# Kernel optimization log

Measured on AMD Instinct MI355X. Metric: run time of the kernel, lower is better.

The kernel has to match this reference:

```python
import jax, jax.numpy as jnp
import numpy as np

B, N, CS, CV, K = 8, 2048, 256, 128, 3
EPS = 1e-6


def _eq_layernorm(s, v):
    # scalars: standard layernorm over channels; vectors: RMS of channel norms (equivariant)
    mu = s.mean(-1, keepdims=True)
    var = ((s - mu) ** 2).mean(-1, keepdims=True)
    s = (s - mu) * jax.lax.rsqrt(var + EPS)
    n2 = (v ** 2).sum(-1).mean(-1, keepdims=True)  # [b,n,1]
    v = v * jax.lax.rsqrt(n2 + EPS)[..., None]
    return s, v


def setup_inputs() -> dict:
    key = jax.random.key(0)
    ks = jax.random.split(key, 7)
    fan_s = K * (CS + CV)       # 1152
    fan_v = K * (CS + 2 * CV)   # 1536
    return {
        "x_s": jax.random.normal(ks[0], (B, N, CS), jnp.float32),
        "x_v": jax.random.normal(ks[1], (B, N, CV, 3), jnp.float32),
        "coords": jax.random.normal(ks[2], (B, N, 3), jnp.float32) * 10.0,
        "W_conv_s": jax.random.normal(ks[3], (fan_s, CS), jnp.float32),
        "W_conv_v": jax.random.normal(ks[4], (fan_v, CV), jnp.float32),
        "W_si_s": jax.random.normal(ks[5], (CS, CS), jnp.float32),
        "W_si_v": jax.random.normal(ks[6], (CV, CV), jnp.float32),
    }


def reference(x_s, x_v, coords, W_conv_s, W_conv_v, W_si_s, W_si_v):
    b, n, cs = x_s.shape
    cv = x_v.shape[2]
    pad = K // 2
    # 'same' padding: zeros for features, edge for coords (zero displacement at boundary)
    sp = jnp.pad(x_s, ((0, 0), (pad, pad), (0, 0)))
    vp = jnp.pad(x_v, ((0, 0), (pad, pad), (0, 0), (0, 0)))
    cp = jnp.pad(coords, ((0, 0), (pad, pad), (0, 0)), mode="edge")
    s_win = jnp.stack([sp[:, k:k + n] for k in range(K)], 2)   # [b,n,K,cs]
    v_win = jnp.stack([vp[:, k:k + n] for k in range(K)], 2)   # [b,n,K,cv,3]
    c_win = jnp.stack([cp[:, k:k + n] for k in range(K)], 2)   # [b,n,K,3]

    d = c_win - coords[:, :, None, :]
    dn = jnp.linalg.norm(d, axis=-1, keepdims=True)
    rhat = d * jnp.where(dn > 1e-6, 1.0 / jnp.maximum(dn, 1e-6), 0.0)

    # Clebsch-Gordan paths of (0e,1e) features with sh = (1, rhat)
    vdot = jnp.einsum("bnkcd,bnkd->bnkc", v_win, rhat)                    # 1x1 -> 0
    scal_in = jnp.concatenate([s_win, vdot], -1).reshape(b, n, -1)        # [b,n,K*(cs+cv)]
    s_rhat = s_win[..., None] * rhat[:, :, :, None, :]                    # 0x1 -> 1
    v_cross = jnp.cross(v_win, rhat[:, :, :, None, :])                    # 1x1 -> 1
    vec_in = jnp.concatenate([v_win, s_rhat, v_cross], 3).reshape(b, n, -1, 3)

    # SequenceConvolution linear mixing (fan-in normalized) + norm=True
    h_s = jnp.einsum("bnp,po->bno", scal_in, W_conv_s) / float(np.sqrt(scal_in.shape[-1]))
    h_v = jnp.einsum("bnpd,po->bnod", vec_in, W_conv_v) / float(np.sqrt(vec_in.shape[2]))
    h_s, h_v = _eq_layernorm(h_s, h_v)

    # SelfInteraction: per-degree channel mixing, residual=True, norm_last=True
    y_s = h_s + h_s @ W_si_s / float(np.sqrt(cs))
    y_v = h_v + jnp.einsum("bncd,co->bnod", h_v, W_si_v) / float(np.sqrt(cv))
    y_s, y_v = _eq_layernorm(y_s, y_v)

    # block Residual + final EquivariantLayerNorm
    z_s, z_v = _eq_layernorm(x_s + y_s, x_v + y_v)
    return z_s, z_v
```

## Files before the change

kernel.cpp:

```cpp
#include <hip/hip_runtime.h>
#include <hip/hip_bf16.h>


typedef __attribute__((ext_vector_type(8))) short short8;
typedef __attribute__((ext_vector_type(4))) float f32x4;
typedef unsigned short u16;

#define B_   8
#define N_   2048
#define EPS_ 1e-6f
#define TB   64

#define OFF_CS 0
#define OFF_V  294912
#define OFF_G  393216
#define OFF_SS 491520
#define OFF_SV 557056

#define MFMA(a,b,c) __builtin_amdgcn_mfma_f32_16x16x32_bf16((a),(b),(c),0,0,0)

__device__ __forceinline__ u16 f2b(float v){ __hip_bfloat16 h=__float2bfloat16(v); return *(u16*)&h; }

__global__ __launch_bounds__(256) void prep_weights(
    const float* __restrict__ Wcs, const float* __restrict__ Wcv,
    const float* __restrict__ Wss, const float* __restrict__ Wsv,
    u16* __restrict__ ws)
{
    const int bid = blockIdx.x;
    const float* src; int N, r0, ld, c0; u16* dst; int tile;
    if (bid < 288)      { src=Wcs; N=256; r0=0; dst=ws+OFF_CS; ld=1152; c0=0; tile=bid; }
    else if (bid < 336) { int k=(bid-288)/16; tile=(bid-288)%16;
                          src=Wcv; N=128; r0=k*512;     dst=ws+OFF_V; ld=768; c0=k*256; }
    else if (bid < 432) { int k=(bid-336)/32; tile=(bid-336)%32;
                          src=Wcv; N=128; r0=k*512+128; dst=ws+OFF_G; ld=768; c0=k*256; }
    else if (bid < 480) { int k=(bid-432)/16; tile=(bid-432)%16;
                          src=Wcv; N=128; r0=k*512+384; dst=ws+OFF_V; ld=768; c0=k*256+128; }
    else if (bid < 544) { tile=bid-480; src=Wss; N=256; r0=0; dst=ws+OFF_SS; ld=256; c0=0; }
    else                { tile=bid-544; src=Wsv; N=128; r0=0; dst=ws+OFF_SV; ld=128; c0=0; }
    const int ntN = N >> 5;
    const int kt = (tile/ntN)*32, nn = (tile%ntN)*32;
    __shared__ float t[32][33];
    const int r = threadIdx.x >> 5, c = threadIdx.x & 31;
#pragma unroll
    for (int i = 0; i < 4; ++i)
        t[r+8*i][c] = src[(size_t)(r0+kt+r+8*i)*N + nn+c];
    __syncthreads();
#pragma unroll
    for (int i = 0; i < 4; ++i)
        dst[(size_t)(nn+r+8*i)*ld + c0+kt+c] = f2b(t[c][r+8*i]);
}

__device__ __forceinline__ void ln_reduce(
    float p1[4][4], float p2[4][4], float pv[4][4], f32x4* red,
    int lm, int lq4, int w, float mu[4][4], float ss[4][4], float vs[4][4])
{
    __syncthreads();
#pragma unroll
    for (int m2 = 1; m2 < 16; m2 <<= 1)
#pragma unroll
        for (int m = 0; m < 4; ++m)
#pragma unroll
            for (int q = 0; q < 4; ++q) {
                p1[m][q] += __shfl_xor(p1[m][q], m2);
                p2[m][q] += __shfl_xor(p2[m][q], m2);
                pv[m][q] += __shfl_xor(pv[m][q], m2);
            }
    if (lm == 0)
#pragma unroll
        for (int m = 0; m < 4; ++m)
#pragma unroll
            for (int q = 0; q < 4; ++q) {
                f32x4 r = {p1[m][q], p2[m][q], pv[m][q], 0.f};
                red[(m*16+lq4+q)*8 + w] = r;
            }
    __syncthreads();
#pragma unroll
    for (int m = 0; m < 4; ++m)
#pragma unroll
        for (int q = 0; q < 4; ++q) {
            const int t = m*16 + lq4 + q;
            f32x4 rs = red[t*8+0];
#pragma unroll
            for (int i = 1; i < 8; ++i) rs += red[t*8+i];
            const float mm = rs.x * (1.f/256.f);
            mu[m][q] = mm;
            ss[m][q] = rsqrtf(rs.y*(1.f/256.f) - mm*mm + EPS_);
            vs[m][q] = rsqrtf(rs.z*(1.f/128.f) + EPS_);
        }
}

__global__ __launch_bounds__(512, 2) void mixing_main(
    const float* __restrict__ x_s, const float* __restrict__ x_v,
    const float* __restrict__ coords, const u16* __restrict__ wt,
    float* __restrict__ out)
{
    __shared__ __align__(16) char smem[162816];
    u16*   fs  = (u16*)smem;
    u16*   fv  = (u16*)(smem + 50176);
    u16*   hsb = (u16*)smem;
    u16*   hvb = (u16*)(smem + 50176);
    float* xvL = (float*)(smem + 50176);
    float* rhp = (float*)(smem + 151552);
    f32x4* red = (f32x4*)(smem + 154624);

    const int tid = threadIdx.x;
    const int w   = tid >> 6, l = tid & 63;
    const int lm  = l & 15, lk8 = (l >> 4) << 3, lq4 = (l >> 4) << 2;
    const int gt0 = blockIdx.x * TB;
    const int n0  = gt0 & (N_ - 1);
    const int seq0 = gt0 - n0;
    const size_t ZV0 = (size_t)B_ * N_ * 256;

    if (tid < 192) {
        const int t = tid / 3, k = tid - 3 * (tid / 3);
        const int jn = n0 + t + k - 1;
        const int jc = jn < 0 ? 0 : (jn > N_-1 ? N_-1 : jn);
        const float* cj = coords + (size_t)(seq0 + jc) * 3;
        const float* c0p = coords + (size_t)(gt0 + t) * 3;
        const float d0 = cj[0]-c0p[0], d1 = cj[1]-c0p[1], d2 = cj[2]-c0p[2];
        const float dn = sqrtf(d0*d0 + d1*d1 + d2*d2);
        const float inv = dn > 1e-6f ? 1.f/dn : 0.f;
        rhp[(t*3+k)*4+0] = d0*inv; rhp[(t*3+k)*4+1] = d1*inv; rhp[(t*3+k)*4+2] = d2*inv;
    }
    __syncthreads();

    const f32x4 fz = {0.f,0.f,0.f,0.f};
    f32x4 acc_s[4][2];
    f32x4 accv[12];
#pragma unroll
    for (int m = 0; m < 4; ++m) { acc_s[m][0] = fz; acc_s[m][1] = fz; }
#pragma unroll
    for (int mi = 0; mi < 12; ++mi) accv[mi] = fz;

    const int bt = tid >> 3;
    const int bx = tid & 7;

#pragma unroll 1
    for (int k = 0; k < 3; ++k) {
        const int jn = n0 + bt + k - 1;
        const bool valid = (unsigned)jn < (unsigned)N_;
        const size_t j = (size_t)seq0 + (valid ? jn : 0);
        {
            const int c0 = bx * 32;
            const float4* sp = (const float4*)(x_s + j*256 + c0);
#pragma unroll
            for (int h = 0; h < 4; ++h) {
                float v[8];
                if (valid) {
                    const float4 f0 = sp[2*h], f1 = sp[2*h+1];
                    v[0]=f0.x; v[1]=f0.y; v[2]=f0.z; v[3]=f0.w;
                    v[4]=f1.x; v[5]=f1.y; v[6]=f1.z; v[7]=f1.w;
                } else {
#pragma unroll
                    for (int i = 0; i < 8; ++i) v[i] = 0.f;
                }
                short8 p;
#pragma unroll
                for (int i = 0; i < 8; ++i) p[i] = (short)f2b(v[i]);
                *(short8*)(fs + bt*392 + c0 + 8*h) = p;
            }
        }
        {
            const int ch0 = bx * 16;
            const float r0 = rhp[(bt*3+k)*4+0];
            const float r1 = rhp[(bt*3+k)*4+1];
            const float r2 = rhp[(bt*3+k)*4+2];
#pragma unroll
            for (int hh = 0; hh < 2; ++hh) {
                const int cb = ch0 + 8*hh;
                float vv[24];
                if (valid) {
                    const float4* vp = (const float4*)(x_v + ((size_t)j*128 + cb)*3);
#pragma unroll
                    for (int i = 0; i < 6; ++i) {
                        const float4 f = vp[i];
                        vv[4*i]=f.x; vv[4*i+1]=f.y; vv[4*i+2]=f.z; vv[4*i+3]=f.w;
                    }
                } else {
#pragma unroll
                    for (int i = 0; i < 24; ++i) vv[i] = 0.f;
                }
                short8 dv, w0, w1, w2, x0, x1, x2;
#pragma unroll
                for (int m = 0; m < 8; ++m) {
                    const float a0 = vv[3*m], a1 = vv[3*m+1], a2 = vv[3*m+2];
                    dv[m] = (short)f2b(a0*r0 + a1*r1 + a2*r2);
                    w0[m] = (short)f2b(a0); w1[m] = (short)f2b(a1); w2[m] = (short)f2b(a2);
                    x0[m] = (short)f2b(a1*r2 - a2*r1);
                    x1[m] = (short)f2b(a2*r0 - a0*r2);
                    x2[m] = (short)f2b(a0*r1 - a1*r0);
                }
                *(short8*)(fs + bt*392 + 256 + cb)            = dv;
                *(short8*)(fv + (0*64+bt)*264 + cb)           = w0;
                *(short8*)(fv + (1*64+bt)*264 + cb)           = w1;
                *(short8*)(fv + (2*64+bt)*264 + cb)           = w2;
                *(short8*)(fv + (0*64+bt)*264 + 128 + cb)     = x0;
                *(short8*)(fv + (1*64+bt)*264 + 128 + cb)     = x1;
                *(short8*)(fv + (2*64+bt)*264 + 128 + cb)     = x2;
            }
        }

        const u16* bS0 = wt + OFF_CS + k*384 + (size_t)((2*w+0)*16+lm)*1152;
        const u16* bS1 = wt + OFF_CS + k*384 + (size_t)((2*w+1)*16+lm)*1152;
        const u16* bGp = wt + OFF_G  + k*256 + (size_t)(w*16+lm)*768;
        const u16* bVp = wt + OFF_V  + k*256 + (size_t)(w*16+lm)*768;
        short8 Bs0[3], Bs1[3], Bg[3], Bv[4];
#pragma unroll
        for (int i = 0; i < 3; ++i) {
            Bs0[i] = *(const short8*)(bS0 + i*32 + lk8);
            Bs1[i] = *(const short8*)(bS1 + i*32 + lk8);
            Bg[i]  = *(const short8*)(bGp + i*32 + lk8);
        }
        __syncthreads();

        f32x4 agc[4] = {fz, fz, fz, fz};
#pragma unroll
        for (int ks = 0; ks < 12; ++ks) {
            const int r = ks % 3;
            const short8 b0 = Bs0[r], b1 = Bs1[r], bg = Bg[r];
            if (ks + 3 < 12) {
                Bs0[r] = *(const short8*)(bS0 + (ks+3)*32 + lk8);
                Bs1[r] = *(const short8*)(bS1 + (ks+3)*32 + lk8);
            }
            if (ks + 3 < 8)
                Bg[r] = *(const short8*)(bGp + (ks+3)*32 + lk8);
            if (ks == 9) {
#pragma unroll
                for (int i = 0; i < 4; ++i)
                    Bv[i] = *(const short8*)(bVp + i*32 + lk8);
            }
            const int ko = ks*32 + lk8;
#pragma unroll
            for (int m = 0; m < 4; ++m) {
                const short8 a = *(const short8*)(fs + (m*16+lm)*392 + ko);
                acc_s[m][0] = MFMA(a, b0, acc_s[m][0]);
                acc_s[m][1] = MFMA(a, b1, acc_s[m][1]);
                if (ks < 8) agc[m] = MFMA(a, bg, agc[m]);
            }
        }
#pragma unroll
        for (int ks = 0; ks < 8; ++ks) {
            const int r = ks & 3;
            const short8 bv = Bv[r];
            if (ks + 4 < 8)
                Bv[r] = *(const short8*)(bVp + (ks+4)*32 + lk8);
            const int ko = ks*32 + lk8;
#pragma unroll
            for (int mi = 0; mi < 12; ++mi) {
                const short8 a = *(const short8*)(
                    fv + ((mi>>2)*64 + (mi&3)*16 + lm)*264 + ko);
                accv[mi] = MFMA(a, bv, accv[mi]);
            }
        }
#pragma unroll
        for (int mi = 0; mi < 12; ++mi) {
            const int m = mi & 3, d = mi >> 2;
#pragma unroll
            for (int q = 0; q < 4; ++q)
                accv[mi][q] += agc[m][q] * rhp[((m*16+lq4+q)*3 + k)*4 + d];
        }
        __syncthreads();
    }

    const float inv_fs = 0.029462783f;
    const float inv_fv = 0.0255155136f;
#pragma unroll
    for (int m = 0; m < 4; ++m)
#pragma unroll
        for (int u = 0; u < 2; ++u)
#pragma unroll
            for (int q = 0; q < 4; ++q) acc_s[m][u][q] *= inv_fs;
#pragma unroll
    for (int mi = 0; mi < 12; ++mi)
#pragma unroll
        for (int q = 0; q < 4; ++q) accv[mi][q] *= inv_fv;

    float p1[4][4], p2[4][4], pv[4][4], mu[4][4], ss[4][4], vs[4][4];
#pragma unroll
    for (int m = 0; m < 4; ++m)
#pragma unroll
        for (int q = 0; q < 4; ++q) {
            float a = 0.f, b = 0.f, c = 0.f;
#pragma unroll
            for (int u = 0; u < 2; ++u) { const float x = acc_s[m][u][q]; a += x; b += x*x; }
#pragma unroll
            for (int d = 0; d < 3; ++d) { const float x = accv[d*4+m][q]; c += x*x; }
            p1[m][q] = a; p2[m][q] = b; pv[m][q] = c;
        }
    ln_reduce(p1, p2, pv, red, lm, lq4, w, mu, ss, vs);

#pragma unroll
    for (int m = 0; m < 4; ++m)
#pragma unroll
        for (int u = 0; u < 2; ++u)
#pragma unroll
            for (int q = 0; q < 4; ++q) {
                const float h = (acc_s[m][u][q] - mu[m][q]) * ss[m][q];
                acc_s[m][u][q] = h;
                hsb[(m*16+lq4+q)*264 + (2*w+u)*16 + lm] = f2b(h);
            }
#pragma unroll
    for (int mi = 0; mi < 12; ++mi)
#pragma unroll
        for (int q = 0; q < 4; ++q) {
            const float h = accv[mi][q] * vs[mi&3][q];
            accv[mi][q] = h;
            hvb[((mi>>2)*64 + (mi&3)*16 + lq4 + q)*136 + w*16 + lm] = f2b(h);
        }

    const u16* bP0 = wt + OFF_SS + (size_t)((2*w+0)*16+lm)*256;
    const u16* bP1 = wt + OFF_SS + (size_t)((2*w+1)*16+lm)*256;
    const u16* bPv = wt + OFF_SV + (size_t)(w*16+lm)*128;
    short8 Cs0[3], Cs1[3], Cv[4];
#pragma unroll
    for (int i = 0; i < 3; ++i) {
        Cs0[i] = *(const short8*)(bP0 + i*32 + lk8);
        Cs1[i] = *(const short8*)(bP1 + i*32 + lk8);
    }
#pragma unroll
    for (int i = 0; i < 4; ++i)
        Cv[i] = *(const short8*)(bPv + i*32 + lk8);
    __syncthreads();

    f32x4 accs[4][2];
    f32x4 accw[12];
#pragma unroll
    for (int m = 0; m < 4; ++m) { accs[m][0] = fz; accs[m][1] = fz; }
#pragma unroll
    for (int mi = 0; mi < 12; ++mi) accw[mi] = fz;
#pragma unroll
    for (int ks = 0; ks < 8; ++ks) {
        const int r = ks % 3;
        const short8 c0 = Cs0[r], c1 = Cs1[r];
        if (ks + 3 < 8) {
            Cs0[r] = *(const short8*)(bP0 + (ks+3)*32 + lk8);
            Cs1[r] = *(const short8*)(bP1 + (ks+3)*32 + lk8);
        }
        const int ko = ks*32 + lk8;
#pragma unroll
        for (int m = 0; m < 4; ++m) {
            const short8 a = *(const short8*)(hsb + (m*16+lm)*264 + ko);
            accs[m][0] = MFMA(a, c0, accs[m][0]);
            accs[m][1] = MFMA(a, c1, accs[m][1]);
        }
    }
#pragma unroll
    for (int ks = 0; ks < 4; ++ks) {
        const int ko = ks*32 + lk8;
#pragma unroll
        for (int mi = 0; mi < 12; ++mi) {
            const short8 a = *(const short8*)(
                hvb + ((mi>>2)*64 + (mi&3)*16 + lm)*136 + ko);
            accw[mi] = MFMA(a, Cv[ks], accw[mi]);
        }
    }

#pragma unroll
    for (int m = 0; m < 4; ++m)
#pragma unroll
        for (int u = 0; u < 2; ++u)
#pragma unroll
            for (int q = 0; q < 4; ++q) acc_s[m][u][q] += accs[m][u][q] * 0.0625f;
#pragma unroll
    for (int mi = 0; mi < 12; ++mi)
#pragma unroll
        for (int q = 0; q < 4; ++q) accv[mi][q] += accw[mi][q] * 0.08838834764f;

#pragma unroll
    for (int m = 0; m < 4; ++m)
#pragma unroll
        for (int q = 0; q < 4; ++q) {
            float a = 0.f, b = 0.f, c = 0.f;
#pragma unroll
            for (int u = 0; u < 2; ++u) { const float x = acc_s[m][u][q]; a += x; b += x*x; }
#pragma unroll
            for (int d = 0; d < 3; ++d) { const float x = accv[d*4+m][q]; c += x*x; }
            p1[m][q] = a; p2[m][q] = b; pv[m][q] = c;
        }
    float4 xr[12];
    {
        const float4* xvsrc = (const float4*)(x_v + (size_t)gt0 * 384);
#pragma unroll
        for (int i = 0; i < 12; ++i) xr[i] = xvsrc[tid + i*512];
    }
    ln_reduce(p1, p2, pv, red, lm, lq4, w, mu, ss, vs);
#pragma unroll
    for (int i = 0; i < 12; ++i) ((float4*)xvL)[tid + i*512] = xr[i];
    __syncthreads();

#pragma unroll
    for (int m = 0; m < 4; ++m)
#pragma unroll
        for (int u = 0; u < 2; ++u)
#pragma unroll
            for (int q = 0; q < 4; ++q)
                acc_s[m][u][q] = (acc_s[m][u][q] - mu[m][q]) * ss[m][q]
                    + x_s[(size_t)(gt0 + m*16 + lq4 + q)*256 + (2*w+u)*16 + lm];
#pragma unroll
    for (int mi = 0; mi < 12; ++mi)
#pragma unroll
        for (int q = 0; q < 4; ++q) {
            const int t = (mi&3)*16 + lq4 + q;
            accv[mi][q] = accv[mi][q] * vs[mi&3][q]
                + xvL[t*384 + (w*16+lm)*3 + (mi>>2)];
        }

#pragma unroll
    for (int m = 0; m < 4; ++m)
#pragma unroll
        for (int q = 0; q < 4; ++q) {
            float a = 0.f, b = 0.f, c = 0.f;
#pragma unroll
            for (int u = 0; u < 2; ++u) { const float x = acc_s[m][u][q]; a += x; b += x*x; }
#pragma unroll
            for (int d = 0; d < 3; ++d) { const float x = accv[d*4+m][q]; c += x*x; }
            p1[m][q] = a; p2[m][q] = b; pv[m][q] = c;
        }
    ln_reduce(p1, p2, pv, red, lm, lq4, w, mu, ss, vs);

#pragma unroll
    for (int m = 0; m < 4; ++m)
#pragma unroll
        for (int u = 0; u < 2; ++u)
#pragma unroll
            for (int q = 0; q < 4; ++q)
                out[(size_t)(gt0 + m*16 + lq4 + q)*256 + (2*w+u)*16 + lm] =
                    (acc_s[m][u][q] - mu[m][q]) * ss[m][q];
#pragma unroll
    for (int mi = 0; mi < 12; ++mi)
#pragma unroll
        for (int q = 0; q < 4; ++q) {
            const int t = (mi&3)*16 + lq4 + q;
            xvL[t*384 + (w*16+lm)*3 + (mi>>2)] = accv[mi][q] * vs[mi&3][q];
        }
    __syncthreads();
    {
        f32x4* dst = (f32x4*)(out + ZV0 + (size_t)gt0 * 384);
        const f32x4* srcv = (const f32x4*)xvL;
#pragma unroll
        for (int i = 0; i < 12; ++i)
            __builtin_nontemporal_store(srcv[tid + i*512], dst + tid + i*512);
    }
}

extern "C" void kernel_launch(void* const* d_in, const int* in_sizes, int n_in,
                              void* d_out, int out_size, void* d_ws, size_t ws_size,
                              hipStream_t stream) {
    const float* x_s    = (const float*)d_in[0];
    const float* x_v    = (const float*)d_in[1];
    const float* coords = (const float*)d_in[2];
    const float* Wcs    = (const float*)d_in[3];
    const float* Wcv    = (const float*)d_in[4];
    const float* Wss    = (const float*)d_in[5];
    const float* Wsv    = (const float*)d_in[6];
    float* out = (float*)d_out;
    u16* ws = (u16*)d_ws;

    hipLaunchKernelGGL(prep_weights, dim3(560), dim3(256), 0, stream,
                       Wcs, Wcv, Wss, Wsv, ws);
    hipLaunchKernelGGL(mixing_main, dim3((B_ * N_) / TB), dim3(512), 0, stream,
                       x_s, x_v, coords, ws, out);
}
```

Measured before the change: 111.8 us.

## Retile vector GEMMs so each wave owns a token quarter and four channel tiles

```diff
diff --git a/kernel.cpp b/kernel.cpp
--- a/kernel.cpp
+++ b/kernel.cpp
@@ -106,6 +106,8 @@
     const int tid = threadIdx.x;
     const int w   = tid >> 6, l = tid & 63;
     const int lm  = l & 15, lk8 = (l >> 4) << 3, lq4 = (l >> 4) << 2;
+    const int tq  = w >> 1;
+    const int ch  = w & 1;
     const int gt0 = blockIdx.x * TB;
     const int n0  = gt0 & (N_ - 1);
     const int seq0 = gt0 - n0;
@@ -126,11 +128,13 @@
 
     const f32x4 fz = {0.f,0.f,0.f,0.f};
     f32x4 acc_s[4][2];
-    f32x4 accv[12];
+    f32x4 accv[3][4];
 #pragma unroll
     for (int m = 0; m < 4; ++m) { acc_s[m][0] = fz; acc_s[m][1] = fz; }
 #pragma unroll
-    for (int mi = 0; mi < 12; ++mi) accv[mi] = fz;
+    for (int d = 0; d < 3; ++d)
+#pragma unroll
+        for (int j = 0; j < 4; ++j) accv[d][j] = fz;
 
     const int bt = tid >> 3;
     const int bx = tid & 7;
@@ -140,34 +144,31 @@
         const int jn = n0 + bt + k - 1;
         const bool valid = (unsigned)jn < (unsigned)N_;
         const size_t j = (size_t)seq0 + (valid ? jn : 0);
+#pragma unroll
+        for (int s = 0; s < 4; ++s) {
+            const int cc = bx*8 + s*64;
+            float v[8];
+            if (valid) {
+                const float4* sp = (const float4*)(x_s + j*256 + cc);
+                const float4 f0 = sp[0], f1 = sp[1];
+                v[0]=f0.x; v[1]=f0.y; v[2]=f0.z; v[3]=f0.w;
+                v[4]=f1.x; v[5]=f1.y; v[6]=f1.z; v[7]=f1.w;
+            } else {
+#pragma unroll
+                for (int i = 0; i < 8; ++i) v[i] = 0.f;
+            }
+            short8 p;
+#pragma unroll
+            for (int i = 0; i < 8; ++i) p[i] = (short)f2b(v[i]);
+            *(short8*)(fs + bt*392 + cc) = p;
+        }
         {
-            const int c0 = bx * 32;
-            const float4* sp = (const float4*)(x_s + j*256 + c0);
-#pragma unroll
-            for (int h = 0; h < 4; ++h) {
-                float v[8];
-                if (valid) {
-                    const float4 f0 = sp[2*h], f1 = sp[2*h+1];
-                    v[0]=f0.x; v[1]=f0.y; v[2]=f0.z; v[3]=f0.w;
-                    v[4]=f1.x; v[5]=f1.y; v[6]=f1.z; v[7]=f1.w;
-                } else {
-#pragma unroll
-                    for (int i = 0; i < 8; ++i) v[i] = 0.f;
-                }
-                short8 p;
-#pragma unroll
-                for (int i = 0; i < 8; ++i) p[i] = (short)f2b(v[i]);
-                *(short8*)(fs + bt*392 + c0 + 8*h) = p;
-            }
-        }
-        {
-            const int ch0 = bx * 16;
             const float r0 = rhp[(bt*3+k)*4+0];
             const float r1 = rhp[(bt*3+k)*4+1];
             const float r2 = rhp[(bt*3+k)*4+2];
 #pragma unroll
             for (int hh = 0; hh < 2; ++hh) {
-                const int cb = ch0 + 8*hh;
+                const int cb = bx*8 + hh*64;
                 float vv[24];
                 if (valid) {
                     const float4* vp = (const float4*)(x_v + ((size_t)j*128 + cb)*3);
@@ -190,75 +191,73 @@
                     x1[m] = (short)f2b(a2*r0 - a0*r2);
                     x2[m] = (short)f2b(a0*r1 - a1*r0);
                 }
-                *(short8*)(fs + bt*392 + 256 + cb)            = dv;
-                *(short8*)(fv + (0*64+bt)*264 + cb)           = w0;
-                *(short8*)(fv + (1*64+bt)*264 + cb)           = w1;
-                *(short8*)(fv + (2*64+bt)*264 + cb)           = w2;
-                *(short8*)(fv + (0*64+bt)*264 + 128 + cb)     = x0;
-                *(short8*)(fv + (1*64+bt)*264 + 128 + cb)     = x1;
-                *(short8*)(fv + (2*64+bt)*264 + 128 + cb)     = x2;
-            }
-        }
-
-        const u16* bS0 = wt + OFF_CS + k*384 + (size_t)((2*w+0)*16+lm)*1152;
-        const u16* bS1 = wt + OFF_CS + k*384 + (size_t)((2*w+1)*16+lm)*1152;
-        const u16* bGp = wt + OFF_G  + k*256 + (size_t)(w*16+lm)*768;
-        const u16* bVp = wt + OFF_V  + k*256 + (size_t)(w*16+lm)*768;
-        short8 Bs0[3], Bs1[3], Bg[3], Bv[4];
-#pragma unroll
-        for (int i = 0; i < 3; ++i) {
-            Bs0[i] = *(const short8*)(bS0 + i*32 + lk8);
-            Bs1[i] = *(const short8*)(bS1 + i*32 + lk8);
-            Bg[i]  = *(const short8*)(bGp + i*32 + lk8);
+                *(short8*)(fs + bt*392 + 256 + cb)        = dv;
+                *(short8*)(fv + (0*64+bt)*264 + cb)       = w0;
+                *(short8*)(fv + (1*64+bt)*264 + cb)       = w1;
+                *(short8*)(fv + (2*64+bt)*264 + cb)       = w2;
+                *(short8*)(fv + (0*64+bt)*264 + 128 + cb) = x0;
+                *(short8*)(fv + (1*64+bt)*264 + 128 + cb) = x1;
+                *(short8*)(fv + (2*64+bt)*264 + 128 + cb) = x2;
+            }
         }
         __syncthreads();
 
+        const u16* rowS0 = wt + OFF_CS + k*384 + (size_t)((2*w+0)*16+lm)*1152;
+        const u16* rowS1 = wt + OFF_CS + k*384 + (size_t)((2*w+1)*16+lm)*1152;
+        const u16* rowG0 = wt + OFF_G + k*256 + (size_t)(ch*64 +  0+lm)*768;
+        const u16* rowG1 = wt + OFF_G + k*256 + (size_t)(ch*64 + 16+lm)*768;
+        const u16* rowG2 = wt + OFF_G + k*256 + (size_t)(ch*64 + 32+lm)*768;
+        const u16* rowG3 = wt + OFF_G + k*256 + (size_t)(ch*64 + 48+lm)*768;
+        const u16* rowV0 = wt + OFF_V + k*256 + (size_t)(ch*64 +  0+lm)*768;
+        const u16* rowV1 = wt + OFF_V + k*256 + (size_t)(ch*64 + 16+lm)*768;
+        const u16* rowV2 = wt + OFF_V + k*256 + (size_t)(ch*64 + 32+lm)*768;
+        const u16* rowV3 = wt + OFF_V + k*256 + (size_t)(ch*64 + 48+lm)*768;
+
         f32x4 agc[4] = {fz, fz, fz, fz};
 #pragma unroll
         for (int ks = 0; ks < 12; ++ks) {
-            const int r = ks % 3;
-            const short8 b0 = Bs0[r], b1 = Bs1[r], bg = Bg[r];
-            if (ks + 3 < 12) {
-                Bs0[r] = *(const short8*)(bS0 + (ks+3)*32 + lk8);
-                Bs1[r] = *(const short8*)(bS1 + (ks+3)*32 + lk8);
-            }
-            if (ks + 3 < 8)
-                Bg[r] = *(const short8*)(bGp + (ks+3)*32 + lk8);
-            if (ks == 9) {
-#pragma unroll
-                for (int i = 0; i < 4; ++i)
-                    Bv[i] = *(const short8*)(bVp + i*32 + lk8);
-            }
             const int ko = ks*32 + lk8;
+            const short8 b0 = *(const short8*)(rowS0 + ko);
+            const short8 b1 = *(const short8*)(rowS1 + ko);
 #pragma unroll
             for (int m = 0; m < 4; ++m) {
                 const short8 a = *(const short8*)(fs + (m*16+lm)*392 + ko);
                 acc_s[m][0] = MFMA(a, b0, acc_s[m][0]);
                 acc_s[m][1] = MFMA(a, b1, acc_s[m][1]);
-                if (ks < 8) agc[m] = MFMA(a, bg, agc[m]);
+            }
+            if (ks < 8) {
+                const short8 ag = *(const short8*)(fs + (tq*16+lm)*392 + ko);
+                agc[0] = MFMA(ag, *(const short8*)(rowG0 + ko), agc[0]);
+                agc[1] = MFMA(ag, *(const short8*)(rowG1 + ko), agc[1]);
+                agc[2] = MFMA(ag, *(const short8*)(rowG2 + ko), agc[2]);
+                agc[3] = MFMA(ag, *(const short8*)(rowG3 + ko), agc[3]);
             }
         }
 #pragma unroll
         for (int ks = 0; ks < 8; ++ks) {
-            const int r = ks & 3;
-            const short8 bv = Bv[r];
-            if (ks + 4 < 8)
-                Bv[r] = *(const short8*)(bVp + (ks+4)*32 + lk8);
             const int ko = ks*32 + lk8;
-#pragma unroll
-            for (int mi = 0; mi < 12; ++mi) {
-                const short8 a = *(const short8*)(
-                    fv + ((mi>>2)*64 + (mi&3)*16 + lm)*264 + ko);
-                accv[mi] = MFMA(a, bv, accv[mi]);
-            }
-        }
-#pragma unroll
-        for (int mi = 0; mi < 12; ++mi) {
-            const int m = mi & 3, d = mi >> 2;
-#pragma unroll
-            for (int q = 0; q < 4; ++q)
-                accv[mi][q] += agc[m][q] * rhp[((m*16+lq4+q)*3 + k)*4 + d];
-        }
+            const short8 bv0 = *(const short8*)(rowV0 + ko);
+            const short8 bv1 = *(const short8*)(rowV1 + ko);
+            const short8 bv2 = *(const short8*)(rowV2 + ko);
+            const short8 bv3 = *(const short8*)(rowV3 + ko);
+#pragma unroll
+            for (int d = 0; d < 3; ++d) {
+                const short8 a = *(const short8*)(fv + (d*64 + tq*16 + lm)*264 + ko);
+                accv[d][0] = MFMA(a, bv0, accv[d][0]);
+                accv[d][1] = MFMA(a, bv1, accv[d][1]);
+                accv[d][2] = MFMA(a, bv2, accv[d][2]);
+                accv[d][3] = MFMA(a, bv3, accv[d][3]);
+            }
+        }
+#pragma unroll
+        for (int d = 0; d < 3; ++d)
+#pragma unroll
+            for (int j2 = 0; j2 < 4; ++j2)
+#pragma unroll
+                for (int q = 0; q < 4; ++q) {
+                    const int t = tq*16 + lq4 + q;
+                    accv[d][j2][q] += agc[j2][q] * rhp[(t*3+k)*4+d];
+                }
         __syncthreads();
     }
 
@@ -271,23 +270,35 @@
 #pragma unroll
             for (int q = 0; q < 4; ++q) acc_s[m][u][q] *= inv_fs;
 #pragma unroll
-    for (int mi = 0; mi < 12; ++mi)
-#pragma unroll
-        for (int q = 0; q < 4; ++q) accv[mi][q] *= inv_fv;
+    for (int d = 0; d < 3; ++d)
+#pragma unroll
+        for (int j2 = 0; j2 < 4; ++j2)
+#pragma unroll
+            for (int q = 0; q < 4; ++q) accv[d][j2][q] *= inv_fv;
 
     float p1[4][4], p2[4][4], pv[4][4], mu[4][4], ss[4][4], vs[4][4];
 #pragma unroll
     for (int m = 0; m < 4; ++m)
 #pragma unroll
         for (int q = 0; q < 4; ++q) {
-            float a = 0.f, b = 0.f, c = 0.f;
+            float a = 0.f, b = 0.f;
 #pragma unroll
             for (int u = 0; u < 2; ++u) { const float x = acc_s[m][u][q]; a += x; b += x*x; }
-#pragma unroll
-            for (int d = 0; d < 3; ++d) { const float x = accv[d*4+m][q]; c += x*x; }
-            p1[m][q] = a; p2[m][q] = b; pv[m][q] = c;
+            p1[m][q] = a; p2[m][q] = b;
+            float c = 0.f;
+            if (m == tq) {
+#pragma unroll
+                for (int d = 0; d < 3; ++d)
+#pragma unroll
+                    for (int j2 = 0; j2 < 4; ++j2) { const float x = accv[d][j2][q]; c += x*x; }
+            }
+            pv[m][q] = c;
         }
     ln_reduce(p1, p2, pv, red, lm, lq4, w, mu, ss, vs);
+    float vst[4];
+#pragma unroll
+    for (int q = 0; q < 4; ++q)
+        vst[q] = (tq==0) ? vs[0][q] : (tq==1) ? vs[1][q] : (tq==2) ? vs[2][q] : vs[3][q];
 
 #pragma unroll
     for (int m = 0; m < 4; ++m)
@@ -300,82 +311,93 @@
                 hsb[(m*16+lq4+q)*264 + (2*w+u)*16 + lm] = f2b(h);
             }
 #pragma unroll
-    for (int mi = 0; mi < 12; ++mi)
+    for (int d = 0; d < 3; ++d)
+#pragma unroll
+        for (int j2 = 0; j2 < 4; ++j2)
+#pragma unroll
+            for (int q = 0; q < 4; ++q) {
+                const float h = accv[d][j2][q] * vst[q];
+                accv[d][j2][q] = h;
+                hvb[(d*64 + tq*16 + lq4 + q)*136 + ch*64 + j2*16 + lm] = f2b(h);
+            }
+    __syncthreads();
+
+    {
+        const u16* rowP0 = wt + OFF_SS + (size_t)((2*w+0)*16+lm)*256;
+        const u16* rowP1 = wt + OFF_SS + (size_t)((2*w+1)*16+lm)*256;
+        f32x4 accs[4][2];
+#pragma unroll
+        for (int m = 0; m < 4; ++m) { accs[m][0] = fz; accs[m][1] = fz; }
+#pragma unroll
+        for (int ks = 0; ks < 8; ++ks) {
+            const int ko = ks*32 + lk8;
+            const short8 c0 = *(const short8*)(rowP0 + ko);
+            const short8 c1 = *(const short8*)(rowP1 + ko);
+#pragma unroll
+            for (int m = 0; m < 4; ++m) {
+                const short8 a = *(const short8*)(hsb + (m*16+lm)*264 + ko);
+                accs[m][0] = MFMA(a, c0, accs[m][0]);
+                accs[m][1] = MFMA(a, c1, accs[m][1]);
+            }
+        }
+#pragma unroll
+        for (int m = 0; m < 4; ++m)
+#pragma unroll
+            for (int u = 0; u < 2; ++u)
+#pragma unroll
+                for (int q = 0; q < 4; ++q) acc_s[m][u][q] += accs[m][u][q] * 0.0625f;
+    }
+    {
+        const u16* rowQ0 = wt + OFF_SV + (size_t)(ch*64 +  0+lm)*128;
+        const u16* rowQ1 = wt + OFF_SV + (size_t)(ch*64 + 16+lm)*128;
+        const u16* rowQ2 = wt + OFF_SV + (size_t)(ch*64 + 32+lm)*128;
+        const u16* rowQ3 = wt + OFF_SV + (size_t)(ch*64 + 48+lm)*128;
+        f32x4 accw[3][4];
+#pragma unroll
+        for (int d = 0; d < 3; ++d)
+#pragma unroll
+            for (int j2 = 0; j2 < 4; ++j2) accw[d][j2] = fz;
+#pragma unroll
+        for (int ks = 0; ks < 4; ++ks) {
+            const int ko = ks*32 + lk8;
+            const short8 c0 = *(const short8*)(rowQ0 + ko);
+            const short8 c1 = *(const short8*)(rowQ1 + ko);
+            const short8 c2 = *(const short8*)(rowQ2 + ko);
+            const short8 c3 = *(const short8*)(rowQ3 + ko);
+#pragma unroll
+            for (int d = 0; d < 3; ++d) {
+                const short8 a = *(const short8*)(hvb + (d*64 + tq*16 + lm)*136 + ko);
+                accw[d][0] = MFMA(a, c0, accw[d][0]);
+                accw[d][1] = MFMA(a, c1, accw[d][1]);
+                accw[d][2] = MFMA(a, c2, accw[d][2]);
+                accw[d][3] = MFMA(a, c3, accw[d][3]);
+            }
+        }
+#pragma unroll
+        for (int d = 0; d < 3; ++d)
+#pragma unroll
+            for (int j2 = 0; j2 < 4; ++j2)
+#pragma unroll
+                for (int q = 0; q < 4; ++q)
+                    accv[d][j2][q] += accw[d][j2][q] * 0.08838834764f;
+    }
+
+#pragma unroll
+    for (int m = 0; m < 4; ++m)
 #pragma unroll
         for (int q = 0; q < 4; ++q) {
-            const float h = accv[mi][q] * vs[mi&3][q];
-            accv[mi][q] = h;
-            hvb[((mi>>2)*64 + (mi&3)*16 + lq4 + q)*136 + w*16 + lm] = f2b(h);
-        }
-
-    const u16* bP0 = wt + OFF_SS + (size_t)((2*w+0)*16+lm)*256;
-    const u16* bP1 = wt + OFF_SS + (size_t)((2*w+1)*16+lm)*256;
-    const u16* bPv = wt + OFF_SV + (size_t)(w*16+lm)*128;
-    short8 Cs0[3], Cs1[3], Cv[4];
-#pragma unroll
-    for (int i = 0; i < 3; ++i) {
-        Cs0[i] = *(const short8*)(bP0 + i*32 + lk8);
-        Cs1[i] = *(const short8*)(bP1 + i*32 + lk8);
-    }
-#pragma unroll
-    for (int i = 0; i < 4; ++i)
-        Cv[i] = *(const short8*)(bPv + i*32 + lk8);
-    __syncthreads();
-
-    f32x4 accs[4][2];
-    f32x4 accw[12];
-#pragma unroll
-    for (int m = 0; m < 4; ++m) { accs[m][0] = fz; accs[m][1] = fz; }
-#pragma unroll
-    for (int mi = 0; mi < 12; ++mi) accw[mi] = fz;
-#pragma unroll
-    for (int ks = 0; ks < 8; ++ks) {
-        const int r = ks % 3;
-        const short8 c0 = Cs0[r], c1 = Cs1[r];
-        if (ks + 3 < 8) {
-            Cs0[r] = *(const short8*)(bP0 + (ks+3)*32 + lk8);
-            Cs1[r] = *(const short8*)(bP1 + (ks+3)*32 + lk8);
-        }
-        const int ko = ks*32 + lk8;
-#pragma unroll
-        for (int m = 0; m < 4; ++m) {
-            const short8 a = *(const short8*)(hsb + (m*16+lm)*264 + ko);
-            accs[m][0] = MFMA(a, c0, accs[m][0]);
-            accs[m][1] = MFMA(a, c1, accs[m][1]);
-        }
-    }
-#pragma unroll
-    for (int ks = 0; ks < 4; ++ks) {
-        const int ko = ks*32 + lk8;
-#pragma unroll
-        for (int mi = 0; mi < 12; ++mi) {
-            const short8 a = *(const short8*)(
-                hvb + ((mi>>2)*64 + (mi&3)*16 + lm)*136 + ko);
-            accw[mi] = MFMA(a, Cv[ks], accw[mi]);
-        }
-    }
-
-#pragma unroll
-    for (int m = 0; m < 4; ++m)
-#pragma unroll
-        for (int u = 0; u < 2; ++u)
-#pragma unroll
-            for (int q = 0; q < 4; ++q) acc_s[m][u][q] += accs[m][u][q] * 0.0625f;
-#pragma unroll
-    for (int mi = 0; mi < 12; ++mi)
-#pragma unroll
-        for (int q = 0; q < 4; ++q) accv[mi][q] += accw[mi][q] * 0.08838834764f;
-
-#pragma unroll
-    for (int m = 0; m < 4; ++m)
-#pragma unroll
-        for (int q = 0; q < 4; ++q) {
-            float a = 0.f, b = 0.f, c = 0.f;
+            float a = 0.f, b = 0.f;
 #pragma unroll
             for (int u = 0; u < 2; ++u) { const float x = acc_s[m][u][q]; a += x; b += x*x; }
-#pragma unroll
-            for (int d = 0; d < 3; ++d) { const float x = accv[d*4+m][q]; c += x*x; }
-            p1[m][q] = a; p2[m][q] = b; pv[m][q] = c;
+            p1[m][q] = a; p2[m][q] = b;
+            float c = 0.f;
+            if (m == tq) {
+#pragma unroll
+                for (int d = 0; d < 3; ++d)
+#pragma unroll
+                    for (int j2 = 0; j2 < 4; ++j2) { const float x = accv[d][j2][q]; c += x*x; }
+            }
+            pv[m][q] = c;
         }
     float4 xr[12];
     {
@@ -385,6 +407,9 @@
     }
     ln_reduce(p1, p2, pv, red, lm, lq4, w, mu, ss, vs);
 #pragma unroll
+    for (int q = 0; q < 4; ++q)
+        vst[q] = (tq==0) ? vs[0][q] : (tq==1) ? vs[1][q] : (tq==2) ? vs[2][q] : vs[3][q];
+#pragma unroll
     for (int i = 0; i < 12; ++i) ((float4*)xvL)[tid + i*512] = xr[i];
     __syncthreads();
 
@@ -397,26 +422,37 @@
                 acc_s[m][u][q] = (acc_s[m][u][q] - mu[m][q]) * ss[m][q]
                     + x_s[(size_t)(gt0 + m*16 + lq4 + q)*256 + (2*w+u)*16 + lm];
 #pragma unroll
-    for (int mi = 0; mi < 12; ++mi)
+    for (int d = 0; d < 3; ++d)
+#pragma unroll
+        for (int j2 = 0; j2 < 4; ++j2)
+#pragma unroll
+            for (int q = 0; q < 4; ++q) {
+                const int t = tq*16 + lq4 + q;
+                accv[d][j2][q] = accv[d][j2][q] * vst[q]
+                    + xvL[t*384 + (ch*64 + j2*16 + lm)*3 + d];
+            }
+
+#pragma unroll
+    for (int m = 0; m < 4; ++m)
 #pragma unroll
         for (int q = 0; q < 4; ++q) {
-            const int t = (mi&3)*16 + lq4 + q;
-            accv[mi][q] = accv[mi][q] * vs[mi&3][q]
-                + xvL[t*384 + (w*16+lm)*3 + (mi>>2)];
-        }
-
-#pragma unroll
-    for (int m = 0; m < 4; ++m)
-#pragma unroll
-        for (int q = 0; q < 4; ++q) {
-            float a = 0.f, b = 0.f, c = 0.f;
+            float a = 0.f, b = 0.f;
 #pragma unroll
             for (int u = 0; u < 2; ++u) { const float x = acc_s[m][u][q]; a += x; b += x*x; }
-#pragma unroll
-            for (int d = 0; d < 3; ++d) { const float x = accv[d*4+m][q]; c += x*x; }
-            p1[m][q] = a; p2[m][q] = b; pv[m][q] = c;
+            p1[m][q] = a; p2[m][q] = b;
+            float c = 0.f;
+            if (m == tq) {
+#pragma unroll
+                for (int d = 0; d < 3; ++d)
+#pragma unroll
+                    for (int j2 = 0; j2 < 4; ++j2) { const float x = accv[d][j2][q]; c += x*x; }
+            }
+            pv[m][q] = c;
         }
     ln_reduce(p1, p2, pv, red, lm, lq4, w, mu, ss, vs);
+#pragma unroll
+    for (int q = 0; q < 4; ++q)
+        vst[q] = (tq==0) ? vs[0][q] : (tq==1) ? vs[1][q] : (tq==2) ? vs[2][q] : vs[3][q];
 
 #pragma unroll
     for (int m = 0; m < 4; ++m)
@@ -427,12 +463,14 @@
                 out[(size_t)(gt0 + m*16 + lq4 + q)*256 + (2*w+u)*16 + lm] =
                     (acc_s[m][u][q] - mu[m][q]) * ss[m][q];
 #pragma unroll
-    for (int mi = 0; mi < 12; ++mi)
-#pragma unroll
-        for (int q = 0; q < 4; ++q) {
-            const int t = (mi&3)*16 + lq4 + q;
-            xvL[t*384 + (w*16+lm)*3 + (mi>>2)] = accv[mi][q] * vs[mi&3][q];
-        }
+    for (int d = 0; d < 3; ++d)
+#pragma unroll
+        for (int j2 = 0; j2 < 4; ++j2)
+#pragma unroll
+            for (int q = 0; q < 4; ++q) {
+                const int t = tq*16 + lq4 + q;
+                xvL[t*384 + (ch*64 + j2*16 + lm)*3 + d] = accv[d][j2][q] * vst[q];
+            }
     __syncthreads();
     {
         f32x4* dst = (f32x4*)(out + ZV0 + (size_t)gt0 * 384);
```

New measurement: 302.0 us. +170.1%, slower.
